# Performance work log

Hardware: AMD Instinct MI355X
Metric: run time of the kernel (lower is better)

The kernel has to match this reference:

```python
import jax, jax.numpy as jnp
import numpy as np

K, N = 1024, 16384


def setup_inputs() -> dict:
    key = jax.random.key(0)
    k1, k2 = jax.random.split(key)
    # event counts per location/time step (non-negative)
    obs = jax.random.randint(k1, (K, N), 0, 5).astype(jnp.float32)
    # excitation matrix, Uniform(0, 0.01) as in the torch init
    halpha = jax.random.uniform(k2, (K, K), dtype=jnp.float32) * 0.01
    # scalar decay parameter, init 2.0
    hbeta = jnp.array([2.0], dtype=jnp.float32)
    return {"obs": obs, "halpha": halpha, "hbeta": hbeta}


def reference(obs, halpha, hbeta):
    # obs: [K, N] event counts; halpha: [K, K]; hbeta: [1]
    K_, N_ = obs.shape
    hmu = obs.mean(axis=1) / 10.0 + 0.01          # [K]
    beta = hbeta[0]
    decay = jnp.exp(-beta)

    # S_t[k] = sum_{tp < t} beta * exp(-(t - tp) * beta) * obs[k, tp]
    # Exponential kernel admits exact recursion: S_{t+1} = e^{-beta} (S_t + beta * obs_t)
    def step(S, obs_t):
        return decay * (S + beta * obs_t), S

    _, S_all = jax.lax.scan(step, jnp.zeros((K_,), obs.dtype), obs.T)  # S_all: [N, K]

    # lam1[k, t] = sum_j halpha[k, j] * S_all[t, j]   (matches mm(halpha, Nt*kernel).sum(1))
    lam1 = jnp.einsum('kj,nj->kn', halpha, S_all)      # [K, N]
    lams = jax.nn.softplus(hmu[:, None] + lam1)        # [K, N]

    loglik = (obs * jnp.log(lams) - lams).sum()
    return loglik, lams
```

## Files before the change

kernel.cpp:

```cpp
#include <hip/hip_runtime.h>

#define KDIM 1024
#define NDIM 16384
#define CHUNKS 256
#define CLEN 64
#define KTILES 16

typedef __bf16 bf16_t;
typedef bf16_t bf16x8 __attribute__((ext_vector_type(8)));
typedef bf16_t bf16x4 __attribute__((ext_vector_type(4)));
typedef float f32x4 __attribute__((ext_vector_type(4)));

__device__ __forceinline__ void gload_lds16(const bf16_t* g, bf16_t* l) {
  __builtin_amdgcn_global_load_lds(
      (const __attribute__((address_space(1))) void*)g,
      (__attribute__((address_space(3))) void*)l, 16, 0, 0);
}

__global__ __launch_bounds__(256) void k_phase1(const float* __restrict__ obs,
                                                const float* __restrict__ hbeta,
                                                float* __restrict__ carry,
                                                float* __restrict__ psum,
                                                const float* __restrict__ A,
                                                bf16_t* __restrict__ Ab,
                                                unsigned char* __restrict__ obs8) {
  if (blockIdx.x >= 1024) {
    size_t i = ((size_t)(blockIdx.x - 1024) * 256 + threadIdx.x) * 4;
    float4 v = *reinterpret_cast<const float4*>(A + i);
    bf16x4 o;
    o[0] = (bf16_t)v.x; o[1] = (bf16_t)v.y; o[2] = (bf16_t)v.z; o[3] = (bf16_t)v.w;
    *reinterpret_cast<bf16x4*>(Ab + i) = o;
    return;
  }
  __shared__ unsigned char s8[256][68];
  int i = threadIdx.x;
  int k = blockIdx.x;
  float beta = hbeta[0];
  float decay = expf(-beta);
  const float* p = obs + (size_t)k * NDIM + i * CLEN;
  float S = 0.f, sum = 0.f;
#pragma unroll
  for (int t = 0; t < CLEN; t += 4) {
    float4 v = *reinterpret_cast<const float4*>(p + t);
    uchar4 u;
    u.x = (unsigned char)v.x; u.y = (unsigned char)v.y;
    u.z = (unsigned char)v.z; u.w = (unsigned char)v.w;
    *reinterpret_cast<uchar4*>(&s8[i][t]) = u;
    S = decay * (S + beta * v.x);
    S = decay * (S + beta * v.y);
    S = decay * (S + beta * v.z);
    S = decay * (S + beta * v.w);
    sum += v.x + v.y + v.z + v.w;
  }
  carry[(size_t)k * CHUNKS + i] = S;
  psum[(size_t)k * CHUNKS + i] = sum;
  __syncthreads();
  unsigned char* po = obs8 + (size_t)k * NDIM;
#pragma unroll
  for (int w = 0; w < 16; ++w) {
    int t = w * 1024 + i * 4;
    int c = t >> 6, off = t & 63;
    *reinterpret_cast<uchar4*>(po + t) = *reinterpret_cast<const uchar4*>(&s8[c][off]);
  }
}

__global__ __launch_bounds__(64) void k_phase2(const float* __restrict__ hbeta,
                                               float* __restrict__ carry,
                                               const float* __restrict__ psum,
                                               float* __restrict__ hmu) {
  int k = blockIdx.x * blockDim.x + threadIdx.x;
  if (k >= KDIM) return;
  float beta = hbeta[0];
  float dL = expf(-beta * (float)CLEN);
  float Cg = 0.f, tot = 0.f;
  float* pc = carry + (size_t)k * CHUNKS;
  const float* pp = psum + (size_t)k * CHUNKS;
  for (int c = 0; c < CHUNKS; ++c) {
    float loc = pc[c];
    pc[c] = Cg;
    Cg = dL * Cg + loc;
    tot += pp[c];
  }
  hmu[k] = tot * (1.0f / NDIM) * 0.1f + 0.01f;
}

__global__ __launch_bounds__(64) void k_phase3(const unsigned char* __restrict__ obs8,
                                               const float* __restrict__ hbeta,
                                               const float* __restrict__ carry,
                                               bf16_t* __restrict__ S_all) {
  int c  = blockIdx.x & (CHUNKS - 1);
  int kb = blockIdx.x >> 8;
  int lane = threadIdx.x;
  float beta = hbeta[0];
  float decay = expf(-beta);
  __shared__ unsigned char s8[64][68];
  __shared__ bf16_t out_s[64][72];
  int k0 = kb * 64, t0 = c * CLEN;
  const unsigned char* base = obs8 + (size_t)k0 * NDIM + t0;
#pragma unroll 4
  for (int w = 0; w < 16; ++w) {
    int r = w * 4 + (lane >> 4), col = (lane & 15) * 4;
    *reinterpret_cast<uchar4*>(&s8[r][col]) =
        *reinterpret_cast<const uchar4*>(base + (size_t)r * NDIM + col);
  }
  __syncthreads();
  float S = carry[(size_t)(k0 + lane) * CHUNKS + c];
#pragma unroll 8
  for (int t = 0; t < CLEN; ++t) {
    out_s[t][lane] = (bf16_t)S;
    S = decay * (S + beta * (float)s8[lane][t]);
  }
  __syncthreads();
#pragma unroll 4
  for (int t = 0; t < CLEN; ++t)
    S_all[(size_t)(t0 + t) * KDIM + k0 + lane] = out_s[t][lane];
}

__global__ __launch_bounds__(512, 2) void k_gemm(const bf16_t* __restrict__ Ab,
                                                 const bf16_t* __restrict__ Bb,
                                                 const float* __restrict__ hmu,
                                                 const unsigned char* __restrict__ obs8,
                                                 float* __restrict__ out) {
  __shared__ bf16_t As[2][256 * 64];
  __shared__ bf16_t Bs[2][256 * 64];
  int tid = threadIdx.x;
  int b = blockIdx.x;
  int lb = (b & 7) * 32 + (b >> 3);
  int kb = lb & 3;
  int tb = lb >> 2;
  int lane = tid & 63, wid = tid >> 6;
  int wm = wid >> 2, wn = wid & 3;
  int r15 = lane & 15, h = lane >> 4;
  f32x4 acc[8][4] = {};

  const bf16_t* gA[4];
  const bf16_t* gB[4];
#pragma unroll
  for (int i = 0; i < 4; ++i) {
    int slot = i * 512 + tid;
    int row = slot >> 3, sp = slot & 7;
    int sl = sp ^ (row & 7);
    gA[i] = Ab + (size_t)(kb * 256 + row) * KDIM + sl * 8;
    gB[i] = Bb + (size_t)(tb * 256 + row) * KDIM + sl * 8;
  }

#define STAGE_A(buf, kkoff) do { \
  _Pragma("unroll") \
  for (int i = 0; i < 4; ++i) \
    gload_lds16(gA[i] + (kkoff), &As[buf][(i * 512 + wid * 64) * 8]); \
} while (0)
#define STAGE_B(buf, kkoff) do { \
  _Pragma("unroll") \
  for (int i = 0; i < 4; ++i) \
    gload_lds16(gB[i] + (kkoff), &Bs[buf][(i * 512 + wid * 64) * 8]); \
} while (0)

#define A_FRAG(mi, sl) (*reinterpret_cast<const bf16x8*>( \
    &As[cur][(wm * 128 + (mi) * 16 + r15) * 64 + ((((sl)) ^ ((wm * 128 + (mi) * 16 + r15) & 7)) * 8)]))
#define B_FRAG(ni, sl) (*reinterpret_cast<const bf16x8*>( \
    &Bs[cur][(wn * 64 + (ni) * 16 + r15) * 64 + ((((sl)) ^ ((wn * 64 + (ni) * 16 + r15) & 7)) * 8)]))

  STAGE_A(0, 0);
  STAGE_B(0, 0);

  int cur = 0;
  for (int kt = 0; kt < KTILES; ++kt) {
    __builtin_amdgcn_sched_barrier(0);
    __builtin_amdgcn_s_barrier();
    if (kt < KTILES - 1) {
      STAGE_A(cur ^ 1, (kt + 1) * 64);
      asm volatile("s_waitcnt vmcnt(4)" ::: "memory");
    } else {
      asm volatile("s_waitcnt vmcnt(0)" ::: "memory");
    }
    __builtin_amdgcn_s_barrier();

    bf16x8 a0[4], a1[4], bf0[4];
#pragma unroll
    for (int m = 0; m < 4; ++m) a0[m] = A_FRAG(m, h);
#pragma unroll
    for (int n = 0; n < 4; ++n) bf0[n] = B_FRAG(n, h);
    __builtin_amdgcn_s_setprio(1);
#pragma unroll
    for (int m = 0; m < 4; ++m)
#pragma unroll
      for (int n = 0; n < 4; ++n)
        acc[m][n] = __builtin_amdgcn_mfma_f32_16x16x32_bf16(a0[m], bf0[n], acc[m][n], 0, 0, 0);
    __builtin_amdgcn_s_setprio(0);
#pragma unroll
    for (int m = 0; m < 4; ++m) a1[m] = A_FRAG(4 + m, h);
    __builtin_amdgcn_s_setprio(1);
#pragma unroll
    for (int m = 0; m < 4; ++m)
#pragma unroll
      for (int n = 0; n < 4; ++n)
        acc[4 + m][n] = __builtin_amdgcn_mfma_f32_16x16x32_bf16(a1[m], bf0[n], acc[4 + m][n], 0, 0, 0);
    __builtin_amdgcn_s_setprio(0);
    if (kt < KTILES - 1) STAGE_B(cur ^ 1, (kt + 1) * 64);
#pragma unroll
    for (int m = 0; m < 4; ++m) a0[m] = A_FRAG(m, 4 + h);
#pragma unroll
    for (int n = 0; n < 4; ++n) bf0[n] = B_FRAG(n, 4 + h);
    __builtin_amdgcn_s_setprio(1);
#pragma unroll
    for (int m = 0; m < 4; ++m)
#pragma unroll
      for (int n = 0; n < 4; ++n)
        acc[m][n] = __builtin_amdgcn_mfma_f32_16x16x32_bf16(a0[m], bf0[n], acc[m][n], 0, 0, 0);
    __builtin_amdgcn_s_setprio(0);
#pragma unroll
    for (int m = 0; m < 4; ++m) a1[m] = A_FRAG(4 + m, 4 + h);
    __builtin_amdgcn_s_setprio(1);
#pragma unroll
    for (int m = 0; m < 4; ++m)
#pragma unroll
      for (int n = 0; n < 4; ++n)
        acc[4 + m][n] = __builtin_amdgcn_mfma_f32_16x16x32_bf16(a1[m], bf0[n], acc[4 + m][n], 0, 0, 0);
    __builtin_amdgcn_s_setprio(0);
    cur ^= 1;
  }
#undef STAGE_A
#undef STAGE_B
#undef A_FRAG
#undef B_FRAG

  float lsum = 0.f;
  float* lams = out + 1;
#pragma unroll
  for (int mi = 0; mi < 8; ++mi) {
    int krow0 = kb * 256 + wm * 128 + mi * 16 + h * 4;
#pragma unroll
    for (int ni = 0; ni < 4; ++ni) {
      int t = tb * 256 + wn * 64 + ni * 16 + r15;
#pragma unroll
      for (int r = 0; r < 4; ++r) {
        int krow = krow0 + r;
        float x = hmu[krow] + acc[mi][ni][r];
        float lam = fmaxf(x, 0.f) + __logf(1.f + __expf(-fabsf(x)));
        lams[(size_t)krow * NDIM + t] = lam;
        float o = (float)obs8[(size_t)krow * NDIM + t];
        lsum += o * __logf(lam) - lam;
      }
    }
  }
  lsum += __shfl_down(lsum, 32);
  lsum += __shfl_down(lsum, 16);
  lsum += __shfl_down(lsum, 8);
  lsum += __shfl_down(lsum, 4);
  lsum += __shfl_down(lsum, 2);
  lsum += __shfl_down(lsum, 1);
  __shared__ float wsum[8];
  if (lane == 0) wsum[wid] = lsum;
  __syncthreads();
  if (tid == 0) {
    float s = 0.f;
#pragma unroll
    for (int w = 0; w < 8; ++w) s += wsum[w];
    atomicAdd(out, s);
  }
}

extern "C" void kernel_launch(void* const* d_in, const int* in_sizes, int n_in,
                              void* d_out, int out_size, void* d_ws, size_t ws_size,
                              hipStream_t stream) {
  const float* obs    = (const float*)d_in[0];
  const float* halpha = (const float*)d_in[1];
  const float* hbeta  = (const float*)d_in[2];
  float* out = (float*)d_out;

  char* ws = (char*)d_ws;
  bf16_t* S_all = (bf16_t*)ws;
  float*  carry = (float*)(ws + (size_t)NDIM * KDIM * 2);
  float*  psum  = carry + (size_t)KDIM * CHUNKS;
  float*  hmu   = psum + (size_t)KDIM * CHUNKS;
  bf16_t* Ab    = (bf16_t*)(hmu + KDIM);
  unsigned char* obs8 = (unsigned char*)(Ab + (size_t)KDIM * KDIM);

  hipMemsetAsync(d_out, 0, sizeof(float), stream);
  k_phase1<<<2048, 256, 0, stream>>>(obs, hbeta, carry, psum, halpha, Ab, obs8);
  k_phase2<<<16, 64, 0, stream>>>(hbeta, carry, psum, hmu);
  k_phase3<<<(KDIM / 64) * CHUNKS, 64, 0, stream>>>(obs8, hbeta, carry, S_all);
  k_gemm<<<4 * (NDIM / 256), 512, 0, stream>>>(Ab, S_all, hmu, obs8, out);
}
```

Measured before the change: 107.2 us.

## Switch GEMM to 4-stage K=32 pipeline with unswizzled LDS tiles

Replaces the double-buffered K=64 tile loop in the GEMM kernel with a four-buffer pipeline of K=32 tiles, prefetching three tiles ahead and loading A and B together. Each iteration loads all fragments at once and issues 32 MFMAs. The XOR swizzle on the LDS layout is dropped, since a 32-wide row is only four 16-byte segments. The aim is to hide global latency better with deeper prefetch, at the cost of twice as many barriers per K and possible LDS bank conflicts on the fragment reads.

Result: slower. 115.4 us (+7.7%).

```diff
diff --git a/kernel.cpp b/kernel.cpp
--- a/kernel.cpp
+++ b/kernel.cpp
@@ -4,7 +4,7 @@
 #define NDIM 16384
 #define CHUNKS 256
 #define CLEN 64
-#define KTILES 16
+#define KT32 32
 
 typedef __bf16 bf16_t;
 typedef bf16_t bf16x8 __attribute__((ext_vector_type(8)));
@@ -121,8 +121,8 @@
                                                  const float* __restrict__ hmu,
                                                  const unsigned char* __restrict__ obs8,
                                                  float* __restrict__ out) {
-  __shared__ bf16_t As[2][256 * 64];
-  __shared__ bf16_t Bs[2][256 * 64];
+  __shared__ bf16_t As[4][256 * 32];
+  __shared__ bf16_t Bs[4][256 * 32];
   int tid = threadIdx.x;
   int b = blockIdx.x;
   int lb = (b & 7) * 32 + (b >> 3);
@@ -133,96 +133,55 @@
   int r15 = lane & 15, h = lane >> 4;
   f32x4 acc[8][4] = {};
 
-  const bf16_t* gA[4];
-  const bf16_t* gB[4];
-#pragma unroll
-  for (int i = 0; i < 4; ++i) {
+  const bf16_t* gA[2];
+  const bf16_t* gB[2];
+#pragma unroll
+  for (int i = 0; i < 2; ++i) {
     int slot = i * 512 + tid;
-    int row = slot >> 3, sp = slot & 7;
-    int sl = sp ^ (row & 7);
+    int row = slot >> 2, sl = slot & 3;
     gA[i] = Ab + (size_t)(kb * 256 + row) * KDIM + sl * 8;
     gB[i] = Bb + (size_t)(tb * 256 + row) * KDIM + sl * 8;
   }
 
-#define STAGE_A(buf, kkoff) do { \
+#define STAGE(tt) do { \
+  int bb = (tt) & 3; \
   _Pragma("unroll") \
-  for (int i = 0; i < 4; ++i) \
-    gload_lds16(gA[i] + (kkoff), &As[buf][(i * 512 + wid * 64) * 8]); \
+  for (int i = 0; i < 2; ++i) { \
+    gload_lds16(gA[i] + (tt) * 32, &As[bb][(i * 512 + wid * 64) * 8]); \
+    gload_lds16(gB[i] + (tt) * 32, &Bs[bb][(i * 512 + wid * 64) * 8]); \
+  } \
 } while (0)
-#define STAGE_B(buf, kkoff) do { \
-  _Pragma("unroll") \
-  for (int i = 0; i < 4; ++i) \
-    gload_lds16(gB[i] + (kkoff), &Bs[buf][(i * 512 + wid * 64) * 8]); \
-} while (0)
-
-#define A_FRAG(mi, sl) (*reinterpret_cast<const bf16x8*>( \
-    &As[cur][(wm * 128 + (mi) * 16 + r15) * 64 + ((((sl)) ^ ((wm * 128 + (mi) * 16 + r15) & 7)) * 8)]))
-#define B_FRAG(ni, sl) (*reinterpret_cast<const bf16x8*>( \
-    &Bs[cur][(wn * 64 + (ni) * 16 + r15) * 64 + ((((sl)) ^ ((wn * 64 + (ni) * 16 + r15) & 7)) * 8)]))
-
-  STAGE_A(0, 0);
-  STAGE_B(0, 0);
-
-  int cur = 0;
-  for (int kt = 0; kt < KTILES; ++kt) {
+
+  STAGE(0);
+  STAGE(1);
+  STAGE(2);
+
+  for (int t = 0; t < KT32; ++t) {
     __builtin_amdgcn_sched_barrier(0);
     __builtin_amdgcn_s_barrier();
-    if (kt < KTILES - 1) {
-      STAGE_A(cur ^ 1, (kt + 1) * 64);
-      asm volatile("s_waitcnt vmcnt(4)" ::: "memory");
-    } else {
-      asm volatile("s_waitcnt vmcnt(0)" ::: "memory");
-    }
+    if (t <= KT32 - 4) STAGE(t + 3);
+    if (t <= KT32 - 3)      asm volatile("s_waitcnt vmcnt(8)" ::: "memory");
+    else if (t == KT32 - 2) asm volatile("s_waitcnt vmcnt(4)" ::: "memory");
+    else                    asm volatile("s_waitcnt vmcnt(0)" ::: "memory");
     __builtin_amdgcn_s_barrier();
 
-    bf16x8 a0[4], a1[4], bf0[4];
-#pragma unroll
-    for (int m = 0; m < 4; ++m) a0[m] = A_FRAG(m, h);
-#pragma unroll
-    for (int n = 0; n < 4; ++n) bf0[n] = B_FRAG(n, h);
+    const int buf = t & 3;
+    bf16x8 a[8], bv[4];
+#pragma unroll
+    for (int mi = 0; mi < 8; ++mi)
+      a[mi] = *reinterpret_cast<const bf16x8*>(&As[buf][(wm * 128 + mi * 16 + r15) * 32 + h * 8]);
+#pragma unroll
+    for (int ni = 0; ni < 4; ++ni)
+      bv[ni] = *reinterpret_cast<const bf16x8*>(&Bs[buf][(wn * 64 + ni * 16 + r15) * 32 + h * 8]);
     __builtin_amdgcn_s_setprio(1);
 #pragma unroll
-    for (int m = 0; m < 4; ++m)
-#pragma unroll
-      for (int n = 0; n < 4; ++n)
-        acc[m][n] = __builtin_amdgcn_mfma_f32_16x16x32_bf16(a0[m], bf0[n], acc[m][n], 0, 0, 0);
+    for (int mi = 0; mi < 8; ++mi)
+#pragma unroll
+      for (int ni = 0; ni < 4; ++ni)
+        acc[mi][ni] = __builtin_amdgcn_mfma_f32_16x16x32_bf16(a[mi], bv[ni], acc[mi][ni], 0, 0, 0);
     __builtin_amdgcn_s_setprio(0);
-#pragma unroll
-    for (int m = 0; m < 4; ++m) a1[m] = A_FRAG(4 + m, h);
-    __builtin_amdgcn_s_setprio(1);
-#pragma unroll
-    for (int m = 0; m < 4; ++m)
-#pragma unroll
-      for (int n = 0; n < 4; ++n)
-        acc[4 + m][n] = __builtin_amdgcn_mfma_f32_16x16x32_bf16(a1[m], bf0[n], acc[4 + m][n], 0, 0, 0);
-    __builtin_amdgcn_s_setprio(0);
-    if (kt < KTILES - 1) STAGE_B(cur ^ 1, (kt + 1) * 64);
-#pragma unroll
-    for (int m = 0; m < 4; ++m) a0[m] = A_FRAG(m, 4 + h);
-#pragma unroll
-    for (int n = 0; n < 4; ++n) bf0[n] = B_FRAG(n, 4 + h);
-    __builtin_amdgcn_s_setprio(1);
-#pragma unroll
-    for (int m = 0; m < 4; ++m)
-#pragma unroll
-      for (int n = 0; n < 4; ++n)
-        acc[m][n] = __builtin_amdgcn_mfma_f32_16x16x32_bf16(a0[m], bf0[n], acc[m][n], 0, 0, 0);
-    __builtin_amdgcn_s_setprio(0);
-#pragma unroll
-    for (int m = 0; m < 4; ++m) a1[m] = A_FRAG(4 + m, 4 + h);
-    __builtin_amdgcn_s_setprio(1);
-#pragma unroll
-    for (int m = 0; m < 4; ++m)
-#pragma unroll
-      for (int n = 0; n < 4; ++n)
-        acc[4 + m][n] = __builtin_amdgcn_mfma_f32_16x16x32_bf16(a1[m], bf0[n], acc[4 + m][n], 0, 0, 0);
-    __builtin_amdgcn_s_setprio(0);
-    cur ^= 1;
-  }
-#undef STAGE_A
-#undef STAGE_B
-#undef A_FRAG
-#undef B_FRAG
+  }
+#undef STAGE
 
   float lsum = 0.f;
   float* lams = out + 1;
```

## Fuse chunk-carry prefix scan and mean into phase1, drop phase2 kernel

Applied to the files above, without the earlier changes.

Phase1 now reads obs rows with coalesced float4 loads across the whole row, writes obs8 directly, and computes per-chunk decay sums from the transposed LDS byte tile. It then runs an in-block Hillis-Steele scan over the 256 chunk carries and a warp-shuffle reduction for the row mean. This removes the serial phase2 kernel (16 blocks with a 256-step loop per row) along with the psum buffer round trip. In exchange it adds many __syncthreads in the scan and a serial 64-step recurrence that reads from LDS.

After: 92.49 us. 13.7% less time.

```diff
diff --git a/kernel.cpp b/kernel.cpp
--- a/kernel.cpp
+++ b/kernel.cpp
@@ -20,7 +20,7 @@
 __global__ __launch_bounds__(256) void k_phase1(const float* __restrict__ obs,
                                                 const float* __restrict__ hbeta,
                                                 float* __restrict__ carry,
-                                                float* __restrict__ psum,
+                                                float* __restrict__ hmu,
                                                 const float* __restrict__ A,
                                                 bf16_t* __restrict__ Ab,
                                                 unsigned char* __restrict__ obs8) {
@@ -33,55 +33,51 @@
     return;
   }
   __shared__ unsigned char s8[256][68];
-  int i = threadIdx.x;
+  __shared__ float sm[256], sa[256];
+  __shared__ float wred[4];
+  int tid = threadIdx.x;
   int k = blockIdx.x;
   float beta = hbeta[0];
   float decay = expf(-beta);
-  const float* p = obs + (size_t)k * NDIM + i * CLEN;
-  float S = 0.f, sum = 0.f;
-#pragma unroll
-  for (int t = 0; t < CLEN; t += 4) {
-    float4 v = *reinterpret_cast<const float4*>(p + t);
+  const float* p = obs + (size_t)k * NDIM;
+  unsigned char* po = obs8 + (size_t)k * NDIM;
+  float sum = 0.f;
+#pragma unroll
+  for (int w = 0; w < 16; ++w) {
+    float4 v = *reinterpret_cast<const float4*>(p + w * 1024 + tid * 4);
+    sum += v.x + v.y + v.z + v.w;
     uchar4 u;
     u.x = (unsigned char)v.x; u.y = (unsigned char)v.y;
     u.z = (unsigned char)v.z; u.w = (unsigned char)v.w;
-    *reinterpret_cast<uchar4*>(&s8[i][t]) = u;
-    S = decay * (S + beta * v.x);
-    S = decay * (S + beta * v.y);
-    S = decay * (S + beta * v.z);
-    S = decay * (S + beta * v.w);
-    sum += v.x + v.y + v.z + v.w;
-  }
-  carry[(size_t)k * CHUNKS + i] = S;
-  psum[(size_t)k * CHUNKS + i] = sum;
-  __syncthreads();
-  unsigned char* po = obs8 + (size_t)k * NDIM;
-#pragma unroll
-  for (int w = 0; w < 16; ++w) {
-    int t = w * 1024 + i * 4;
-    int c = t >> 6, off = t & 63;
-    *reinterpret_cast<uchar4*>(po + t) = *reinterpret_cast<const uchar4*>(&s8[c][off]);
-  }
-}
-
-__global__ __launch_bounds__(64) void k_phase2(const float* __restrict__ hbeta,
-                                               float* __restrict__ carry,
-                                               const float* __restrict__ psum,
-                                               float* __restrict__ hmu) {
-  int k = blockIdx.x * blockDim.x + threadIdx.x;
-  if (k >= KDIM) return;
-  float beta = hbeta[0];
+    *reinterpret_cast<uchar4*>(po + w * 1024 + tid * 4) = u;
+    int c = w * 16 + (tid >> 4), t = 4 * (tid & 15);
+    *reinterpret_cast<uchar4*>(&s8[c][t]) = u;
+  }
+  __syncthreads();
+  float S = 0.f;
+#pragma unroll 8
+  for (int t = 0; t < CLEN; ++t)
+    S = decay * (S + beta * (float)s8[tid][t]);
   float dL = expf(-beta * (float)CLEN);
-  float Cg = 0.f, tot = 0.f;
-  float* pc = carry + (size_t)k * CHUNKS;
-  const float* pp = psum + (size_t)k * CHUNKS;
-  for (int c = 0; c < CHUNKS; ++c) {
-    float loc = pc[c];
-    pc[c] = Cg;
-    Cg = dL * Cg + loc;
-    tot += pp[c];
-  }
-  hmu[k] = tot * (1.0f / NDIM) * 0.1f + 0.01f;
+  sm[tid] = dL; sa[tid] = S;
+  __syncthreads();
+#pragma unroll
+  for (int s = 1; s < 256; s <<= 1) {
+    float mp = 0.f, ap = 0.f;
+    bool act = (tid >= s);
+    if (act) { mp = sm[tid - s]; ap = sa[tid - s]; }
+    __syncthreads();
+    if (act) { sa[tid] += sm[tid] * ap; sm[tid] *= mp; }
+    __syncthreads();
+  }
+  carry[(size_t)k * CHUNKS + tid] = (tid == 0) ? 0.f : sa[tid - 1];
+  sum += __shfl_down(sum, 32); sum += __shfl_down(sum, 16);
+  sum += __shfl_down(sum, 8);  sum += __shfl_down(sum, 4);
+  sum += __shfl_down(sum, 2);  sum += __shfl_down(sum, 1);
+  if ((tid & 63) == 0) wred[tid >> 6] = sum;
+  __syncthreads();
+  if (tid == 0)
+    hmu[k] = (wred[0] + wred[1] + wred[2] + wred[3]) * (1.0f / NDIM) * 0.1f + 0.01f;
 }
 
 __global__ __launch_bounds__(64) void k_phase3(const unsigned char* __restrict__ obs8,
@@ -271,14 +267,12 @@
   char* ws = (char*)d_ws;
   bf16_t* S_all = (bf16_t*)ws;
   float*  carry = (float*)(ws + (size_t)NDIM * KDIM * 2);
-  float*  psum  = carry + (size_t)KDIM * CHUNKS;
-  float*  hmu   = psum + (size_t)KDIM * CHUNKS;
+  float*  hmu   = carry + (size_t)KDIM * CHUNKS;
   bf16_t* Ab    = (bf16_t*)(hmu + KDIM);
   unsigned char* obs8 = (unsigned char*)(Ab + (size_t)KDIM * KDIM);
 
   hipMemsetAsync(d_out, 0, sizeof(float), stream);
-  k_phase1<<<2048, 256, 0, stream>>>(obs, hbeta, carry, psum, halpha, Ab, obs8);
-  k_phase2<<<16, 64, 0, stream>>>(hbeta, carry, psum, hmu);
+  k_phase1<<<2048, 256, 0, stream>>>(obs, hbeta, carry, hmu, halpha, Ab, obs8);
   k_phase3<<<(KDIM / 64) * CHUNKS, 64, 0, stream>>>(obs8, hbeta, carry, S_all);
   k_gemm<<<4 * (NDIM / 256), 512, 0, stream>>>(Ab, S_all, hmu, obs8, out);
 }
```
